# Kernel optimization log

Hardware: AMD Instinct MI355X
Metric: run time of the kernel (lower is better)

Reference implementation:

```python
import jax, jax.numpy as jnp
import numpy as np

N = 4096      # number of mesh points
H = 64        # hidden_dim
K = 15        # k_neighbors
E = 32768     # explicit input edges


def _knn_edges(points, k):
    # dense pairwise squared distances [N,N]; exclude self via +inf diagonal
    sq = jnp.sum(points * points, axis=1)
    d2 = sq[:, None] - 2.0 * (points @ points.T) + sq[None, :]
    n = points.shape[0]
    d2 = d2.at[jnp.arange(n), jnp.arange(n)].set(jnp.inf)
    _, idx = jax.lax.top_k(-d2, k)              # [N,k] nearest neighbor ids
    src = jnp.repeat(jnp.arange(n), k)          # node i
    dst = idx.reshape(-1)                       # its neighbors
    return src, dst


def setup_inputs() -> dict:
    key = jax.random.key(0)
    ks = jax.random.split(key, 8)
    points = jax.random.normal(ks[0], (N, 3), jnp.float32)
    features = jax.random.normal(ks[1], (N, H), jnp.float32)
    edge_index = jax.random.randint(ks[2], (2, E), 0, N)

    def lin(k, fin, fout):
        k1, k2 = jax.random.split(k)
        s = 1.0 / np.sqrt(fin)
        W = jax.random.uniform(k1, (fout, fin), jnp.float32, -s, s)
        b = jax.random.uniform(k2, (fout,), jnp.float32, -s, s)
        return W, b

    W_theta, b_theta = lin(ks[3], 3, H)
    W_phi, b_phi = lin(ks[4], H, H)
    W_q, b_q = lin(ks[5], H, H)
    W_k, b_k = lin(ks[6], H, H)
    return dict(points=points, features=features, edge_index=edge_index,
                W_theta=W_theta, b_theta=b_theta, W_phi=W_phi, b_phi=b_phi,
                W_q=W_q, b_q=b_q, W_k=W_k, b_k=b_k)


def reference(points, features, edge_index, W_theta, b_theta, W_phi, b_phi,
              W_q, b_q, W_k, b_k):
    n = points.shape[0]
    # extended edge list = explicit edges + KNN edges (src = node, dst = neighbor)
    src_knn, dst_knn = _knn_edges(points, K)
    src = jnp.concatenate([edge_index[0], src_knn])
    dst = jnp.concatenate([edge_index[1], dst_knn])

    # per-node max-pooled edge MLP: max_j W_theta(p_j - p_i), then ReLU(W_phi(.))
    diff = points[dst] - points[src]                     # [M,3]
    h = diff @ W_theta.T + b_theta                       # [M,H]
    max_feat = jax.ops.segment_max(h, src, num_segments=n)  # [N,H] (every node has >=K nbrs)
    dev = jax.nn.relu(max_feat @ W_phi.T + b_phi)        # [N,H]

    # edge softmax attention: attn[i,j] = exp(q_j . k_i) / sum_{j' in N(i)} exp(q_j' . k_i)
    q = dev @ W_q.T + b_q
    kk = dev @ W_k.T + b_k
    e = jnp.exp(jnp.sum(q[dst] * kk[src], axis=-1))      # [M]
    denom = jax.ops.segment_sum(e, src, num_segments=n)  # [N]
    attn = jnp.zeros((n, n), e.dtype).at[src, dst].set(e / denom[src])

    # dense adjacency and sparsified adjacency A_s = attn @ A @ attn^T
    A = jnp.zeros((n, n), points.dtype).at[src, dst].set(1.0)
    A_s = attn @ A @ attn.T
    return A_s
```

## Files before the change

### kernel.cpp

```cpp
#include <hip/hip_runtime.h>

#define NN 4096
#define HD 64
#define KNB 15
#define NE 32768
#define NM (NE + NN*KNB)
#define W64 (NN/64)
#define RB 4
#define MAXH 96
#define NCH (NN/64)
#define TDP 65

typedef unsigned long long u64;
typedef unsigned int u32;

__device__ __forceinline__ u32 fmapu(float f) {
  int i = __float_as_int(f);
  return (u32)(i ^ ((i >> 31) | 0x80000000));
}

__device__ __forceinline__ float dot64(const float* __restrict__ a,
                                       const float* __restrict__ b) {
  const float4* a4 = (const float4*)a;
  const float4* b4 = (const float4*)b;
  float s = 0.f;
#pragma unroll
  for (int t = 0; t < 16; ++t) {
    float4 x = a4[t], y = b4[t];
    s = fmaf(x.x, y.x, s); s = fmaf(x.y, y.y, s);
    s = fmaf(x.z, y.z, s); s = fmaf(x.w, y.w, s);
  }
  return s;
}

__device__ __forceinline__ void edge_decode(int m, const int* __restrict__ ei,
                                            const int* __restrict__ knn_idx,
                                            int& s, int& d) {
  if (m < NE) { s = ei[m]; d = ei[NE + m]; }
  else { int mm = m - NE; s = mm / KNB; d = knn_idx[mm]; }
}

__global__ __launch_bounds__(256) void knn_kernel(const float* __restrict__ pts,
                                                  int* __restrict__ knn_idx,
                                                  u32* __restrict__ zero_base,
                                                  int zero_n) {
  int zi = blockIdx.x * 256 + threadIdx.x;
  if (zi < zero_n) zero_base[zi] = 0u;

  __shared__ int hist[4][256];
  __shared__ int s_eq[256];
  __shared__ u32 s_cnt[2];
  __shared__ int s_bin, s_below, s_need;
  int i = blockIdx.x;
  int tid = threadIdx.x;
  int lane = tid & 63, wv = tid >> 6;
  float px = pts[i*3+0], py = pts[i*3+1], pz = pts[i*3+2];
  float sqi = __fadd_rn(__fadd_rn(__fmul_rn(px,px), __fmul_rn(py,py)), __fmul_rn(pz,pz));
  u32 key[16];
#pragma unroll
  for (int s = 0; s < 16; ++s) {
    int j = s*256 + tid;
    float x = pts[j*3+0], y = pts[j*3+1], z = pts[j*3+2];
    float sqj = __fadd_rn(__fadd_rn(__fmul_rn(x,x), __fmul_rn(y,y)), __fmul_rn(z,z));
    float dot = fmaf(pz, z, fmaf(py, y, __fmul_rn(px, x)));
    float d2 = __fadd_rn(__fsub_rn(sqi, __fmul_rn(2.0f, dot)), sqj);
    key[s] = (j == i) ? 0xFFFFFFFFu : fmapu(d2);
  }
  if (tid == 0) s_need = KNB;
  u32 prefix = 0u;
#pragma unroll
  for (int r = 0; r < 4; ++r) {
    int shift = 24 - 8*r;
    for (int t = tid; t < 1024; t += 256) ((int*)hist)[t] = 0;
    __syncthreads();
    u32 mask_hi = (r == 0) ? 0u : (0xFFFFFFFFu << (shift + 8));
#pragma unroll
    for (int s = 0; s < 16; ++s) {
      if ((key[s] & mask_hi) == prefix)
        atomicAdd(&hist[wv][(key[s] >> shift) & 255], 1);
    }
    __syncthreads();
    if (tid < 64) {
      int b0 = tid * 4;
      int c0 = hist[0][b0  ]+hist[1][b0  ]+hist[2][b0  ]+hist[3][b0  ];
      int c1 = hist[0][b0+1]+hist[1][b0+1]+hist[2][b0+1]+hist[3][b0+1];
      int c2 = hist[0][b0+2]+hist[1][b0+2]+hist[2][b0+2]+hist[3][b0+2];
      int c3 = hist[0][b0+3]+hist[1][b0+3]+hist[2][b0+3]+hist[3][b0+3];
      int need = s_need;
      int tot = c0 + c1 + c2 + c3;
      int x = tot;
#pragma unroll
      for (int o = 1; o < 64; o <<= 1) {
        int v = __shfl_up(x, o, 64);
        if (tid >= o) x += v;
      }
      int cum = x - tot;
      if (need > cum && need <= cum + c0) { s_bin = b0;   s_below = cum; }
      cum += c0;
      if (need > cum && need <= cum + c1) { s_bin = b0+1; s_below = cum; }
      cum += c1;
      if (need > cum && need <= cum + c2) { s_bin = b0+2; s_below = cum; }
      cum += c2;
      if (need > cum && need <= cum + c3) { s_bin = b0+3; s_below = cum; }
    }
    __syncthreads();
    prefix |= (u32)s_bin << shift;
    if (tid == 0) s_need = s_need - s_below;
  }
  u32 tau = prefix;
  if (tid == 0) { s_cnt[0] = 0u; s_cnt[1] = 0u; }
  __syncthreads();
#pragma unroll
  for (int s = 0; s < 16; ++s) {
    int j = s*256 + tid;
    if (key[s] < tau) {
      u32 p = atomicAdd(&s_cnt[0], 1u);
      knn_idx[i*KNB + p] = j;
    } else if (key[s] == tau) {
      u32 p = atomicAdd(&s_cnt[1], 1u);
      if (p < 256u) s_eq[p] = j;
    }
  }
  __syncthreads();
  if (tid == 0) {
    int cls = (int)s_cnt[0];
    int ceq = (int)s_cnt[1]; if (ceq > 256) ceq = 256;
    int need = KNB - cls;
    for (int r = 0; r < need; ++r) {
      int best = 1 << 30, bidx = 0;
      for (int t = 0; t < ceq; ++t) {
        int v = s_eq[t];
        if (v < best) { best = v; bidx = t; }
      }
      s_eq[bidx] = 1 << 30;
      knn_idx[i*KNB + cls + r] = best;
    }
  }
}

__global__ void bitmap_kernel(const int* __restrict__ ei, const int* __restrict__ knn_idx,
                              u64* __restrict__ bR) {
  int m = blockIdx.x * 256 + threadIdx.x;
  if (m >= NM) return;
  int s, d; edge_decode(m, ei, knn_idx, s, d);
  atomicOr(&bR[(size_t)s*W64 + (d >> 6)], 1ull << (d & 63));
}

__global__ __launch_bounds__(512) void theta_devqk_kernel(const float* __restrict__ pts,
    const u64* __restrict__ bR, int* __restrict__ deg, uint2* __restrict__ cvT,
    const float* __restrict__ Wt, const float* __restrict__ bt,
    const float* __restrict__ Wp, const float* __restrict__ bp,
    const float* __restrict__ Wq, const float* __restrict__ bq,
    const float* __restrict__ Wk, const float* __restrict__ bk,
    float* __restrict__ qv, float* __restrict__ kv) {
  __shared__ float Wps[HD*TDP], Wqs[HD*TDP], Wks[HD*TDP];
  __shared__ float mf[8][HD];
  __shared__ float dv[8][HD];
  __shared__ int colbuf[8][MAXH];
  int tid = threadIdx.x;
  for (int m = tid; m < HD*HD; m += 512) {
    int row = m >> 6, col = m & 63;
    Wps[row*TDP + col] = Wp[m];
    Wqs[row*TDP + col] = Wq[m];
    Wks[row*TDP + col] = Wk[m];
  }
  int lane = tid & 63, sub = tid >> 6;
  int i = blockIdx.x * 8 + sub;
  u64 word = bR[(size_t)i*W64 + lane];
  int cnt = __popcll(word);
  int x = cnt;
#pragma unroll
  for (int o = 1; o < 64; o <<= 1) {
    int v = __shfl_up(x, o, 64);
    if (lane >= o) x += v;
  }
  int rank = x - cnt;
  int degi = __shfl(x, 63, 64);
  if (lane == 63) deg[i] = x;
  int ci = i >> 6, il = i & 63;
  u32* colTx = (u32*)cvT;
  int slot = rank;
  u64 wtmp = word;
  while (wtmp) {
    int b = __builtin_ctzll(wtmp); wtmp &= wtmp - 1;
    int col = lane*64 + b;
    colbuf[sub][slot] = col;
    colTx[(((size_t)(ci*MAXH + slot) << 6) + il) << 1] = (u32)col;
    ++slot;
  }
  __syncthreads();
  float w0 = Wt[lane*3+0], w1 = Wt[lane*3+1], w2 = Wt[lane*3+2], bb = bt[lane];
  float px = pts[i*3+0], py = pts[i*3+1], pz = pts[i*3+2];
  float m = -INFINITY;
  for (int e = 0; e < degi; ++e) {
    int d = colbuf[sub][e];
    float dx = __fsub_rn(pts[d*3+0], px);
    float dy = __fsub_rn(pts[d*3+1], py);
    float dz = __fsub_rn(pts[d*3+2], pz);
    float t = fmaf(dz, w2, fmaf(dy, w1, __fmul_rn(dx, w0)));
    m = fmaxf(m, __fadd_rn(t, bb));
  }
  mf[sub][lane] = m;
  __syncthreads();
  float a = 0.f;
#pragma unroll
  for (int t = 0; t < HD; ++t) a = fmaf(Wps[lane*TDP + t], mf[sub][t], a);
  float dvv = a + bp[lane];
  dv[sub][lane] = dvv > 0.f ? dvv : 0.f;
  __syncthreads();
  float aq = 0.f, ak = 0.f;
#pragma unroll
  for (int t = 0; t < HD; ++t) {
    float xv = dv[sub][t];
    aq = fmaf(Wqs[lane*TDP + t], xv, aq);
    ak = fmaf(Wks[lane*TDP + t], xv, ak);
  }
  qv[(size_t)i*HD + lane] = aq + bq[lane];
  kv[(size_t)i*HD + lane] = ak + bk[lane];
}

#define DENOM_BLKS ((NM + 255) / 256)
#define ELL_BLKS   (NCH * MAXH * 64 / 256)
__global__ void vals_kernel(const int* __restrict__ ei, const int* __restrict__ knn_idx,
    const int* __restrict__ deg,
    const float* __restrict__ qv, const float* __restrict__ kv,
    float* __restrict__ denom, uint2* __restrict__ cvT) {
  if ((int)blockIdx.x < DENOM_BLKS) {
    int m = blockIdx.x * 256 + threadIdx.x;
    if (m >= NM) return;
    int s, d; edge_decode(m, ei, knn_idx, s, d);
    float e = expf(dot64(qv + (size_t)d*HD, kv + (size_t)s*HD));
    atomicAdd(&denom[s], e);
  } else {
    int t = (blockIdx.x - DENOM_BLKS) * 256 + threadIdx.x;
    int c = t / (MAXH * 64);
    int r = t - c * (MAXH * 64);
    int s = r >> 6, jl = r & 63;
    int j = c * 64 + jl;
    if (s >= deg[j]) return;
    u32 l = ((const u32*)cvT)[(size_t)t << 1];
    float sc = dot64(qv + (size_t)l*HD, kv + (size_t)j*HD);
    ((u32*)cvT)[((size_t)t << 1) + 1] = __float_as_uint(expf(sc));
  }
}

__global__ __launch_bounds__(1024, 8) void final_kernel(
    const int* __restrict__ deg, const uint2* __restrict__ cvT,
    const float* __restrict__ denom, float* __restrict__ out) {
  __shared__ float4 T4[NN];
  int tid = threadIdx.x;
  int i0 = blockIdx.x * RB;
  float4 z4 = make_float4(0.f, 0.f, 0.f, 0.f);
  for (int t = tid; t < NN; t += 1024) T4[t] = z4;
  __syncthreads();
  int w = tid >> 6, lane = tid & 63;
  float* Tf = (float*)T4;
  const u32* colTx = (const u32*)cvT;
  {
    int r = w & (RB - 1);
    int i = i0 + r;
    int ci = i >> 6, il = i & 63;
    int degi = deg[i];
    for (int idx = (w >> 2); idx < degi; idx += RB) {
      uint2 e = cvT[((size_t)(ci*MAXH + idx) << 6) + il];
      int k = (int)e.x; float wv = __uint_as_float(e.y);
      int ck = k >> 6, kl = k & 63;
      int degk = deg[k];
      for (int t = lane; t < degk; t += 64) {
        u32 l = colTx[(((size_t)(ck*MAXH + t) << 6) + kl) << 1];
        atomicAdd(&Tf[(int)l * 4 + r], wv);
      }
    }
  }
  __syncthreads();
  float acc[4][RB];
#pragma unroll
  for (int g = 0; g < 4; ++g)
#pragma unroll
    for (int r = 0; r < RB; ++r) acc[g][r] = 0.f;
#pragma unroll
  for (int g = 0; g < 4; ++g) {
    int j = tid + g * 1024;
    int c = j >> 6;
    int dj = deg[j];
    const uint2* p = cvT + ((size_t)(c*MAXH) << 6) + (j & 63);
    int s = 0;
    for (; s + 4 <= dj; s += 4) {
      uint2 e0 = p[(size_t)(s+0) << 6];
      uint2 e1 = p[(size_t)(s+1) << 6];
      uint2 e2 = p[(size_t)(s+2) << 6];
      uint2 e3 = p[(size_t)(s+3) << 6];
      float4 t0 = T4[(int)e0.x];
      float4 t1 = T4[(int)e1.x];
      float4 t2 = T4[(int)e2.x];
      float4 t3 = T4[(int)e3.x];
      float v0 = __uint_as_float(e0.y), v1 = __uint_as_float(e1.y);
      float v2 = __uint_as_float(e2.y), v3 = __uint_as_float(e3.y);
      acc[g][0] = fmaf(v0, t0.x, acc[g][0]); acc[g][1] = fmaf(v0, t0.y, acc[g][1]);
      acc[g][2] = fmaf(v0, t0.z, acc[g][2]); acc[g][3] = fmaf(v0, t0.w, acc[g][3]);
      acc[g][0] = fmaf(v1, t1.x, acc[g][0]); acc[g][1] = fmaf(v1, t1.y, acc[g][1]);
      acc[g][2] = fmaf(v1, t1.z, acc[g][2]); acc[g][3] = fmaf(v1, t1.w, acc[g][3]);
      acc[g][0] = fmaf(v2, t2.x, acc[g][0]); acc[g][1] = fmaf(v2, t2.y, acc[g][1]);
      acc[g][2] = fmaf(v2, t2.z, acc[g][2]); acc[g][3] = fmaf(v2, t2.w, acc[g][3]);
      acc[g][0] = fmaf(v3, t3.x, acc[g][0]); acc[g][1] = fmaf(v3, t3.y, acc[g][1]);
      acc[g][2] = fmaf(v3, t3.z, acc[g][2]); acc[g][3] = fmaf(v3, t3.w, acc[g][3]);
    }
    for (; s < dj; ++s) {
      uint2 e = p[(size_t)s << 6];
      float v = __uint_as_float(e.y);
      float4 tv = T4[(int)e.x];
      acc[g][0] = fmaf(v, tv.x, acc[g][0]);
      acc[g][1] = fmaf(v, tv.y, acc[g][1]);
      acc[g][2] = fmaf(v, tv.z, acc[g][2]);
      acc[g][3] = fmaf(v, tv.w, acc[g][3]);
    }
  }
  float rden[RB];
#pragma unroll
  for (int r = 0; r < RB; ++r) rden[r] = 1.0f / denom[i0 + r];
#pragma unroll
  for (int g = 0; g < 4; ++g) {
    int j = tid + g * 1024;
    float dj_den = denom[j];
#pragma unroll
    for (int r = 0; r < RB; ++r)
      out[(size_t)(i0 + r) * NN + j] = acc[g][r] * rden[r] / dj_den;
  }
}

extern "C" void kernel_launch(void* const* d_in, const int* in_sizes, int n_in,
                              void* d_out, int out_size, void* d_ws, size_t ws_size,
                              hipStream_t stream) {
  (void)in_sizes; (void)n_in; (void)out_size;
  const float* pts = (const float*)d_in[0];
  const int* ei = (const int*)d_in[2];
  const float* Wt = (const float*)d_in[3];
  const float* bt = (const float*)d_in[4];
  const float* Wp = (const float*)d_in[5];
  const float* bp = (const float*)d_in[6];
  const float* Wq = (const float*)d_in[7];
  const float* bq = (const float*)d_in[8];
  const float* Wk = (const float*)d_in[9];
  const float* bk = (const float*)d_in[10];
  float* out = (float*)d_out;

  char* w = (char*)d_ws;
  u64* bR = (u64*)w;        w += (size_t)NN*W64*8;
  float* denom = (float*)w; w += (size_t)NN*4;
  float* qv = (float*)w;    w += (size_t)NN*HD*4;
  float* kv = (float*)w;    w += (size_t)NN*HD*4;
  int* knn_idx = (int*)w;   w += (size_t)NN*KNB*4;
  int* deg = (int*)w;       w += (size_t)NN*4;
  uint2* cvT = (uint2*)w;   w += (size_t)NCH*MAXH*64*8;
  if ((size_t)(w - (char*)d_ws) > ws_size) return;

  int zero_u32s = (int)(((size_t)NN*W64*8 + (size_t)NN*4) / 4);
  hipLaunchKernelGGL(knn_kernel, dim3(NN), dim3(256), 0, stream,
                     pts, knn_idx, (u32*)d_ws, zero_u32s);
  hipLaunchKernelGGL(bitmap_kernel, dim3((NM+255)/256), dim3(256), 0, stream,
                     ei, knn_idx, bR);
  hipLaunchKernelGGL(theta_devqk_kernel, dim3(NN/8), dim3(512), 0, stream,
                     pts, bR, deg, cvT, Wt, bt, Wp, bp, Wq, bq, Wk, bk, qv, kv);
  hipLaunchKernelGGL(vals_kernel, dim3(DENOM_BLKS + ELL_BLKS), dim3(256), 0, stream,
                     ei, knn_idx, deg, qv, kv, denom, cvT);
  hipLaunchKernelGGL(final_kernel, dim3(NN/RB), dim3(1024), 0, stream,
                     deg, cvT, denom, out);
}
```

Before: 184.4 us.

## Replace radix-select KNN with iterative wave-min selection and write bitmap rows directly

Swaps the 4-pass radix histogram top-k selection for 15 rounds of packed 64-bit (distance,index) min reductions, using wave shuffles followed by a cross-wave shared-memory combine. Each KNN block then writes its node's full adjacency bitmap row directly. This removes the global zeroing of the bitmap and the KNN-edge atomics from bitmap_kernel, which now only handles the explicit edges. The cost is 15 block-wide barriers and reductions per node instead of 4 histogram passes. Tie-breaking by lower index is kept through the packed key.

```diff
diff --git a/kernel.cpp b/kernel.cpp
--- a/kernel.cpp
+++ b/kernel.cpp
@@ -19,6 +19,12 @@
   return (u32)(i ^ ((i >> 31) | 0x80000000));
 }
 
+__device__ __forceinline__ u64 shfl_xor_u64(u64 v, int off) {
+  int lo = __shfl_xor((int)(v & 0xFFFFFFFFull), off, 64);
+  int hi = __shfl_xor((int)(v >> 32), off, 64);
+  return ((u64)(u32)hi << 32) | (u32)lo;
+}
+
 __device__ __forceinline__ float dot64(const float* __restrict__ a,
                                        const float* __restrict__ b) {
   const float4* a4 = (const float4*)a;
@@ -42,21 +48,21 @@
 
 __global__ __launch_bounds__(256) void knn_kernel(const float* __restrict__ pts,
                                                   int* __restrict__ knn_idx,
+                                                  u64* __restrict__ bR,
                                                   u32* __restrict__ zero_base,
                                                   int zero_n) {
   int zi = blockIdx.x * 256 + threadIdx.x;
   if (zi < zero_n) zero_base[zi] = 0u;
 
-  __shared__ int hist[4][256];
-  __shared__ int s_eq[256];
-  __shared__ u32 s_cnt[2];
-  __shared__ int s_bin, s_below, s_need;
+  __shared__ u64 sm[KNB][4];
+  __shared__ u64 s_mask[64];
+  __shared__ int s_j[KNB];
   int i = blockIdx.x;
   int tid = threadIdx.x;
   int lane = tid & 63, wv = tid >> 6;
   float px = pts[i*3+0], py = pts[i*3+1], pz = pts[i*3+2];
   float sqi = __fadd_rn(__fadd_rn(__fmul_rn(px,px), __fmul_rn(py,py)), __fmul_rn(pz,pz));
-  u32 key[16];
+  u64 lk[16];
 #pragma unroll
   for (int s = 0; s < 16; ++s) {
     int j = s*256 + tid;
@@ -64,85 +70,51 @@
     float sqj = __fadd_rn(__fadd_rn(__fmul_rn(x,x), __fmul_rn(y,y)), __fmul_rn(z,z));
     float dot = fmaf(pz, z, fmaf(py, y, __fmul_rn(px, x)));
     float d2 = __fadd_rn(__fsub_rn(sqi, __fmul_rn(2.0f, dot)), sqj);
-    key[s] = (j == i) ? 0xFFFFFFFFu : fmapu(d2);
-  }
-  if (tid == 0) s_need = KNB;
-  u32 prefix = 0u;
-#pragma unroll
-  for (int r = 0; r < 4; ++r) {
-    int shift = 24 - 8*r;
-    for (int t = tid; t < 1024; t += 256) ((int*)hist)[t] = 0;
+    u32 key = (j == i) ? 0xFFFFFFFFu : fmapu(d2);
+    lk[s] = ((u64)key << 32) | (u32)j;
+  }
+  u64 lmin = lk[0];
+#pragma unroll
+  for (int s = 1; s < 16; ++s) lmin = (lk[s] < lmin) ? lk[s] : lmin;
+
+  for (int r = 0; r < KNB; ++r) {
+    u64 v = lmin;
+#pragma unroll
+    for (int off = 32; off >= 1; off >>= 1) {
+      u64 o = shfl_xor_u64(v, off);
+      if (o < v) v = o;
+    }
+    if (lane == 0) sm[r][wv] = v;
     __syncthreads();
-    u32 mask_hi = (r == 0) ? 0u : (0xFFFFFFFFu << (shift + 8));
-#pragma unroll
-    for (int s = 0; s < 16; ++s) {
-      if ((key[s] & mask_hi) == prefix)
-        atomicAdd(&hist[wv][(key[s] >> shift) & 255], 1);
-    }
-    __syncthreads();
-    if (tid < 64) {
-      int b0 = tid * 4;
-      int c0 = hist[0][b0  ]+hist[1][b0  ]+hist[2][b0  ]+hist[3][b0  ];
-      int c1 = hist[0][b0+1]+hist[1][b0+1]+hist[2][b0+1]+hist[3][b0+1];
-      int c2 = hist[0][b0+2]+hist[1][b0+2]+hist[2][b0+2]+hist[3][b0+2];
-      int c3 = hist[0][b0+3]+hist[1][b0+3]+hist[2][b0+3]+hist[3][b0+3];
-      int need = s_need;
-      int tot = c0 + c1 + c2 + c3;
-      int x = tot;
-#pragma unroll
-      for (int o = 1; o < 64; o <<= 1) {
-        int v = __shfl_up(x, o, 64);
-        if (tid >= o) x += v;
-      }
-      int cum = x - tot;
-      if (need > cum && need <= cum + c0) { s_bin = b0;   s_below = cum; }
-      cum += c0;
-      if (need > cum && need <= cum + c1) { s_bin = b0+1; s_below = cum; }
-      cum += c1;
-      if (need > cum && need <= cum + c2) { s_bin = b0+2; s_below = cum; }
-      cum += c2;
-      if (need > cum && need <= cum + c3) { s_bin = b0+3; s_below = cum; }
-    }
-    __syncthreads();
-    prefix |= (u32)s_bin << shift;
-    if (tid == 0) s_need = s_need - s_below;
-  }
-  u32 tau = prefix;
-  if (tid == 0) { s_cnt[0] = 0u; s_cnt[1] = 0u; }
-  __syncthreads();
-#pragma unroll
-  for (int s = 0; s < 16; ++s) {
-    int j = s*256 + tid;
-    if (key[s] < tau) {
-      u32 p = atomicAdd(&s_cnt[0], 1u);
-      knn_idx[i*KNB + p] = j;
-    } else if (key[s] == tau) {
-      u32 p = atomicAdd(&s_cnt[1], 1u);
-      if (p < 256u) s_eq[p] = j;
-    }
-  }
-  __syncthreads();
-  if (tid == 0) {
-    int cls = (int)s_cnt[0];
-    int ceq = (int)s_cnt[1]; if (ceq > 256) ceq = 256;
-    int need = KNB - cls;
-    for (int r = 0; r < need; ++r) {
-      int best = 1 << 30, bidx = 0;
-      for (int t = 0; t < ceq; ++t) {
-        int v = s_eq[t];
-        if (v < best) { best = v; bidx = t; }
-      }
-      s_eq[bidx] = 1 << 30;
-      knn_idx[i*KNB + cls + r] = best;
-    }
-  }
-}
-
-__global__ void bitmap_kernel(const int* __restrict__ ei, const int* __restrict__ knn_idx,
-                              u64* __restrict__ bR) {
+    u64 bm = sm[r][0];
+    if (sm[r][1] < bm) bm = sm[r][1];
+    if (sm[r][2] < bm) bm = sm[r][2];
+    if (sm[r][3] < bm) bm = sm[r][3];
+    int j = (int)(u32)(bm & 0xFFFFFFFFull);
+    if (tid == 0) { knn_idx[i*KNB + r] = j; s_j[r] = j; }
+    int owner = j & 255, sid = j >> 8;
+    if (tid == owner) {
+#pragma unroll
+      for (int s2 = 0; s2 < 16; ++s2) if (s2 == sid) lk[s2] = ~0ull;
+    }
+    lmin = lk[0];
+#pragma unroll
+    for (int s2 = 1; s2 < 16; ++s2) lmin = (lk[s2] < lmin) ? lk[s2] : lmin;
+  }
+  if (tid < 64) s_mask[tid] = 0ull;
+  __syncthreads();
+  if (tid < KNB) {
+    int j = s_j[tid];
+    atomicOr(&s_mask[j >> 6], 1ull << (j & 63));
+  }
+  __syncthreads();
+  if (tid < 64) bR[(size_t)i*W64 + tid] = s_mask[tid];
+}
+
+__global__ void bitmap_kernel(const int* __restrict__ ei, u64* __restrict__ bR) {
   int m = blockIdx.x * 256 + threadIdx.x;
-  if (m >= NM) return;
-  int s, d; edge_decode(m, ei, knn_idx, s, d);
+  if (m >= NE) return;
+  int s = ei[m], d = ei[NE + m];
   atomicOr(&bR[(size_t)s*W64 + (d >> 6)], 1ull << (d & 63));
 }
 
@@ -354,11 +326,10 @@
   uint2* cvT = (uint2*)w;   w += (size_t)NCH*MAXH*64*8;
   if ((size_t)(w - (char*)d_ws) > ws_size) return;
 
-  int zero_u32s = (int)(((size_t)NN*W64*8 + (size_t)NN*4) / 4);
   hipLaunchKernelGGL(knn_kernel, dim3(NN), dim3(256), 0, stream,
-                     pts, knn_idx, (u32*)d_ws, zero_u32s);
-  hipLaunchKernelGGL(bitmap_kernel, dim3((NM+255)/256), dim3(256), 0, stream,
-                     ei, knn_idx, bR);
+                     pts, knn_idx, bR, (u32*)denom, NN);
+  hipLaunchKernelGGL(bitmap_kernel, dim3((NE+255)/256), dim3(256), 0, stream,
+                     ei, bR);
   hipLaunchKernelGGL(theta_devqk_kernel, dim3(NN/8), dim3(512), 0, stream,
                      pts, bR, deg, cvT, Wt, bt, Wp, bp, Wq, bq, Wk, bk, qv, kv);
   hipLaunchKernelGGL(vals_kernel, dim3(DENOM_BLKS + ELL_BLKS), dim3(256), 0, stream,
```

Result: faster. 177.7 us (-3.6%).
